# Performance work log

Measured on AMD Instinct MI355X. Metric: run time of the kernel, lower is better.

Reference implementation:

```python
import jax, jax.numpy as jnp
import numpy as np
from jax import lax
jax.config.update("jax_enable_x64", True)

FNV_OFF = np.int64(-3750763034362895579)
FNV_PRIME = np.int64(4294967731)
I64_MAX = np.iinfo(np.int64).max
INF = np.float32(1e38)
CHUNK = 512  # cluster-chunk size for the cdist fallback


def _pack_key(b, c, vx, vy, vz):
    # five-word FNV-1a 64-bit hash with natural int64 wraparound
    h = jnp.full(b.shape, FNV_OFF, dtype=jnp.int64)
    for w in (b, c, vx, vy, vz):
        h = (h ^ w.astype(jnp.int64)) * FNV_PRIME
    return h


def _safe_norm(x):
    s = jnp.sum(x * x, axis=1)
    n = jnp.sqrt(jnp.where(s > 0, s, 1.0))
    return jnp.where(s > 0, n, 0.0)


def setup_inputs() -> dict:
    key = jax.random.key(0)
    k1, k2, k3, k4 = jax.random.split(key, 4)
    N = 65536
    grid = jax.random.randint(k1, (N, 3), 0, 400).astype(jnp.float32)
    batch_id = jnp.sort(jax.random.randint(k2, (N,), 0, 2).astype(jnp.int64))
    label = jax.random.randint(k3, (N,), 0, 8).astype(jnp.int64)
    pred_off = jax.random.normal(k4, (N, 3), dtype=jnp.float32)
    return {"pred_off": pred_off, "grid": grid, "label": label, "batch_id": batch_id,
            "base_grid": 16, "num_cls": 8, "num_batch": 2}


def _forward(pred_off, grid, label, batch_id, base_grid, num_cls, num_batch):
    N = grid.shape[0]
    grid_f = grid.astype(jnp.float32)
    vox = jnp.floor(grid_f / base_grid).astype(jnp.int64)  # [N,3]

    # voxel_grid: bucket by (batch, voxel) -> consecutive cluster ids via unique
    ckey = ((batch_id * 1024 + vox[:, 0]) * 1024 + vox[:, 1]) * 1024 + vox[:, 2]
    _, cluster = jnp.unique(ckey, return_inverse=True, size=N, fill_value=I64_MAX)
    cluster = cluster.reshape(-1)

    # cluster stats (segment scatter-reduce, num_segments = N upper bound)
    cnt = jax.ops.segment_sum(jnp.ones((N,), jnp.float32), cluster, num_segments=N)
    cl_center = jax.ops.segment_sum(grid_f, cluster, num_segments=N) / jnp.maximum(cnt, 1.0)[:, None]
    cl_batch = jax.ops.segment_min(batch_id, cluster, num_segments=N)
    cl_lbl_lo = jax.ops.segment_min(label, cluster, num_segments=N)
    cl_lbl_hi = jax.ops.segment_max(label, cluster, num_segments=N)
    cl_vox = jax.ops.segment_min(vox, cluster, num_segments=N)
    valid_cl = cnt > 0
    pure_cl = (cl_lbl_lo == cl_lbl_hi) & valid_cl
    pure_pt = pure_cl[cluster]

    # hash table of pure clusters, sorted by key (invalid -> sentinel, sorts last)
    pk_all = jnp.where(pure_cl, _pack_key(cl_batch, cl_lbl_lo, cl_vox[:, 0], cl_vox[:, 1], cl_vox[:, 2]), I64_MAX)
    order = jnp.argsort(pk_all)
    pk_sort = pk_all[order]
    pc_sort = cl_center[order]
    ok_sort = pure_cl[order]

    # per (batch,label) global centers
    key_bl = batch_id * num_cls + label
    nbl = num_batch * num_cls
    cnt_bl = jax.ops.segment_sum(jnp.ones((N,), jnp.float32), key_bl, num_segments=nbl)
    global_c = jax.ops.segment_sum(grid_f, key_bl, num_segments=nbl) / jnp.maximum(cnt_bl, 1.0)[:, None]
    step_sign = jnp.sign(global_c[key_bl] - cl_center[cluster]).astype(jnp.int64)  # [N,3]

    # +/-1 and +/-2 voxel hash lookup (steps 1 and K+1=2)
    def probe(step):
        cv = cl_vox[cluster] + step_sign * step
        ck = _pack_key(batch_id, label, cv[:, 0], cv[:, 1], cv[:, 2])
        idx = jnp.searchsorted(pk_sort, ck)
        idxc = jnp.minimum(idx, N - 1)
        hit = (idx < N) & ok_sort[idxc] & (pk_sort[idxc] == ck)
        return hit, pc_sort[idxc]

    hit1, t1 = probe(1)
    hit2, t2 = probe(2)
    hit_pt = hit1 | hit2
    tgt_c = jnp.where(hit1[:, None], t1, jnp.where(hit2[:, None], t2, grid_f))

    # fallback: nearest pure-cluster center with same (batch,label), chunked cdist+argmin
    miss = (~pure_pt) & (~hit_pt)
    code_y = key_bl
    code_x = jnp.where(pure_cl, cl_batch * num_cls + cl_lbl_lo, jnp.int64(-1))
    p2 = jnp.sum(grid_f * grid_f, axis=1)  # [N]

    def body(carry, i):
        best_d, best_c = carry
        c = lax.dynamic_slice_in_dim(cl_center, i * CHUNK, CHUNK)   # [S,3]
        cc = lax.dynamic_slice_in_dim(code_x, i * CHUNK, CHUNK)      # [S]
        d2 = p2[:, None] - 2.0 * (grid_f @ c.T) + jnp.sum(c * c, axis=1)[None, :]  # [N,S]
        d2 = jnp.where(cc[None, :] == code_y[:, None], d2, INF)
        j = jnp.argmin(d2, axis=1)
        dmin = jnp.take_along_axis(d2, j[:, None], axis=1)[:, 0]
        upd = dmin < best_d
        best_d = jnp.where(upd, dmin, best_d)
        best_c = jnp.where(upd[:, None], c[j], best_c)
        return (best_d, best_c), None

    nchunk = N // CHUNK
    (best_d, best_c), _ = lax.scan(body, (jnp.full((N,), INF, jnp.float32), grid_f), jnp.arange(nchunk))
    tgt_c = jnp.where((miss & (best_d < INF))[:, None], best_c, tgt_c)

    # loss: smooth-L1 on offsets below 99th-percentile magnitude + direction cosine loss
    tgt_off = tgt_c - grid_f
    mag = _safe_norm(tgt_off)
    thresh = jnp.quantile(mag, 0.99)
    m1 = mag <= thresh
    d = pred_off - tgt_off
    ad = jnp.abs(d)
    hub = jnp.where(ad < 1.0, 0.5 * d * d, ad - 0.5)
    n1 = jnp.sum(m1).astype(jnp.float32)
    loss_l1 = jnp.where(n1 > 0, jnp.sum(hub * m1[:, None]) / jnp.maximum(n1 * 3.0, 1.0), 0.0)

    md = (mag > 0) & m1
    eps = 1e-4
    pn = _safe_norm(pred_off)
    cos = jnp.sum(pred_off * tgt_off, axis=1) / jnp.maximum(pn * mag, eps)
    nmd = jnp.sum(md).astype(jnp.float32)
    loss_dir = jnp.where(nmd > 0, 1.0 - jnp.sum(cos * md) / jnp.maximum(nmd, 1.0), 0.0)
    return jnp.stack([loss_l1.astype(jnp.float32), loss_dir.astype(jnp.float32)])


def reference(pred_off, grid, label, batch_id, base_grid, num_cls, num_batch):
    return _forward(pred_off, grid, label, batch_id, base_grid, num_cls, num_batch)
```

## Files before the change

### kernel.cpp

```cpp
#include <hip/hip_runtime.h>
#include <climits>

#define VOXD 25
#define SLOT3 (VOXD*VOXD*VOXD)
#define SLOTS (2*SLOT3)
#define NCLS 8
#define NCODE 16
#define NBLK ((SLOTS + 255) / 256)
#define HB 2048
#define FBK 64
#define GSZ 16
#define MPB (256 / GSZ)
#define CSTRIDE SLOT3

struct Scalars {
  double hub;
  double cosSum;
  int n1;
  int nmd;
  int binA, rA, binB, rB;
  float thresh;
  int done;
};

__device__ __forceinline__ int voxslot(int b, int vx, int vy, int vz) {
  return ((b * VOXD + vx) * VOXD + vy) * VOXD + vz;
}

__device__ __forceinline__ int block_scan_i(int v, int* ws, int* total) {
  int lane = threadIdx.x & 63, w = threadIdx.x >> 6;
  int s = v;
  #pragma unroll
  for (int off = 1; off < 64; off <<= 1) {
    int t = __shfl_up(s, off, 64);
    if (lane >= off) s += t;
  }
  if (lane == 63) ws[w] = s;
  __syncthreads();
  if (threadIdx.x < 16) {
    int x = ws[threadIdx.x];
    #pragma unroll
    for (int off = 1; off < 16; off <<= 1) {
      int t = __shfl_up(x, off, 64);
      if (lane >= off) x += t;
    }
    ws[threadIdx.x] = x;
  }
  __syncthreads();
  if (w > 0) s += ws[w - 1];
  *total = ws[15];
  __syncthreads();
  return s;
}

__global__ void k_scatter(const float* __restrict__ grid, const int* __restrict__ label,
                          const int* __restrict__ batch,
                          unsigned long long* vA, unsigned long long* vB, int* lmask,
                          int* blCnt, float* blSum, int n) {
  __shared__ int sCnt[NCODE];
  __shared__ float sSum[3 * NCODE];
  int tid = threadIdx.x;
  if (tid < NCODE) sCnt[tid] = 0;
  if (tid < 3 * NCODE) sSum[tid] = 0.f;
  __syncthreads();
  int i = blockIdx.x * blockDim.x + tid;
  if (i < n) {
    float gx = grid[3*i], gy = grid[3*i+1], gz = grid[3*i+2];
    int ix = (int)gx, iy = (int)gy, iz = (int)gz;
    int vx = (int)floorf(gx * (1.0f/16.0f));
    int vy = (int)floorf(gy * (1.0f/16.0f));
    int vz = (int)floorf(gz * (1.0f/16.0f));
    int b = batch[i], l = label[i];
    int s = voxslot(b, vx, vy, vz);
    atomicAdd(&vA[s], ((unsigned long long)(unsigned)ix << 32) | (unsigned)iy);
    atomicAdd(&vB[s], ((unsigned long long)(unsigned)iz << 24) | 1ULL);
    atomicOr(&lmask[s], 1 << l);
    int bl = b * NCLS + l;
    atomicAdd(&sCnt[bl], 1);
    atomicAdd(&sSum[3*bl], gx); atomicAdd(&sSum[3*bl+1], gy); atomicAdd(&sSum[3*bl+2], gz);
  }
  __syncthreads();
  if (tid < NCODE && sCnt[tid] != 0) atomicAdd(&blCnt[tid], sCnt[tid]);
  if (tid < 3 * NCODE && sSum[tid] != 0.f) atomicAdd(&blSum[tid], sSum[tid]);
}

__global__ void k_prep(const unsigned long long* vA, const unsigned long long* vB,
                       const int* lmask, float4* ctr, float4* pC, int* pSlot,
                       int* codeCnt) {
  __shared__ int lc[NCODE];
  __shared__ int lb[NCODE];
  int tid = threadIdx.x;
  if (tid < NCODE) lc[tid] = 0;
  __syncthreads();
  int s = blockIdx.x * 256 + tid;
  int code = -1, lpos = 0;
  float4 v = make_float4(0.f, 0.f, 0.f, __int_as_float(-2));
  if (s < SLOTS) {
    unsigned long long bq = vB[s];
    unsigned c = (unsigned)(bq & 0xFFFFFFULL);
    if (c > 0) {
      unsigned long long aq = vA[s];
      float fc = (float)c;
      float cx = __fdiv_rn((float)(unsigned)(aq >> 32), fc);
      float cy = __fdiv_rn((float)(unsigned)(aq & 0xFFFFFFFFULL), fc);
      float cz = __fdiv_rn((float)(unsigned)(bq >> 24), fc);
      int m = lmask[s];
      bool pure = (m & (m - 1)) == 0;
      int lbl = __ffs(m) - 1;
      v = make_float4(cx, cy, cz, __int_as_float(pure ? lbl : -1));
      if (pure) {
        code = (s / SLOT3) * NCLS + lbl;
        lpos = atomicAdd(&lc[code], 1);
      }
    }
    ctr[s] = v;
  }
  __syncthreads();
  if (tid < NCODE) lb[tid] = (lc[tid] > 0) ? atomicAdd(&codeCnt[tid], lc[tid]) : 0;
  __syncthreads();
  if (code >= 0) {
    int pos = code * CSTRIDE + lb[code] + lpos;
    float c2 = __fadd_rn(__fadd_rn(__fmul_rn(v.x,v.x), __fmul_rn(v.y,v.y)),
                         __fmul_rn(v.z,v.z));
    pC[pos] = make_float4(v.x, v.y, v.z, c2);
    pSlot[pos] = s;
  }
}

__global__ void k_targets(const float* __restrict__ grid, const int* __restrict__ label,
                          const int* __restrict__ batch,
                          const float4* __restrict__ ctr,
                          const int* __restrict__ blCnt, const float* __restrict__ blSum,
                          float* tgt, float* mag, int* ghist,
                          int* missPart, int* missCnt, int mstride, int n) {
  __shared__ int wCnt[4][NCODE];
  __shared__ int gBase[NCODE];
  __shared__ int h[HB];
  int tid = threadIdx.x, lane = tid & 63, w = tid >> 6;
  for (int t = tid; t < HB; t += 256) h[t] = 0;
  __syncthreads();
  int i = blockIdx.x * blockDim.x + tid;
  bool active = (i < n);
  bool miss = false;
  int mcode = -1;

  if (active) {
    float gx = grid[3*i], gy = grid[3*i+1], gz = grid[3*i+2];
    int vx = (int)floorf(gx * (1.0f/16.0f));
    int vy = (int)floorf(gy * (1.0f/16.0f));
    int vz = (int)floorf(gz * (1.0f/16.0f));
    int b = batch[i], l = label[i];
    int s = voxslot(b, vx, vy, vz);

    float4 own = ctr[s];
    bool purept = (__float_as_int(own.w) >= 0);

    int bl = b * NCLS + l;
    float fbc = (float)max(blCnt[bl], 1);
    float gcx = __fdiv_rn(blSum[3*bl],   fbc);
    float gcy = __fdiv_rn(blSum[3*bl+1], fbc);
    float gcz = __fdiv_rn(blSum[3*bl+2], fbc);

    float dx = __fsub_rn(gcx, own.x);
    float dy = __fsub_rn(gcy, own.y);
    float dz = __fsub_rn(gcz, own.z);
    int sgx = (dx > 0.f) ? 1 : ((dx < 0.f) ? -1 : 0);
    int sgy = (dy > 0.f) ? 1 : ((dy < 0.f) ? -1 : 0);
    int sgz = (dz > 0.f) ? 1 : ((dz < 0.f) ? -1 : 0);

    int ax1 = vx + sgx,     ay1 = vy + sgy,     az1 = vz + sgz;
    int ax2 = vx + 2 * sgx, ay2 = vy + 2 * sgy, az2 = vz + 2 * sgz;
    bool v1 = (unsigned)ax1 < (unsigned)VOXD && (unsigned)ay1 < (unsigned)VOXD &&
              (unsigned)az1 < (unsigned)VOXD;
    bool v2 = (unsigned)ax2 < (unsigned)VOXD && (unsigned)ay2 < (unsigned)VOXD &&
              (unsigned)az2 < (unsigned)VOXD;

    float4 q1 = make_float4(0.f, 0.f, 0.f, __int_as_float(-3));
    float4 q2 = q1;
    if (v1) q1 = ctr[voxslot(b, ax1, ay1, az1)];
    if (v2) q2 = ctr[voxslot(b, ax2, ay2, az2)];

    bool hit1 = v1 && (__float_as_int(q1.w) == l);
    bool hit2 = v2 && (__float_as_int(q2.w) == l);
    bool hit = hit1 || hit2;

    float tx = hit1 ? q1.x : (hit2 ? q2.x : gx);
    float ty = hit1 ? q1.y : (hit2 ? q2.y : gy);
    float tz = hit1 ? q1.z : (hit2 ? q2.z : gz);

    tgt[3*i] = tx; tgt[3*i+1] = ty; tgt[3*i+2] = tz;
    miss = (!purept && !hit);
    if (miss) {
      mcode = bl;
    } else {
      float tox = __fsub_rn(tx, gx), toy = __fsub_rn(ty, gy), toz = __fsub_rn(tz, gz);
      float ssq = __fadd_rn(__fadd_rn(__fmul_rn(tox,tox), __fmul_rn(toy,toy)),
                            __fmul_rn(toz,toz));
      float m = (ssq > 0.f) ? sqrtf(ssq) : 0.f;
      mag[i] = m;
      atomicAdd(&h[__float_as_uint(m) >> 21], 1);
    }
  }
  int myrank = 0;
  #pragma unroll
  for (int c = 0; c < NCODE; ++c) {
    unsigned long long mb = __ballot(mcode == c);
    if (lane == 0) wCnt[w][c] = __popcll(mb);
    if (mcode == c) myrank = __popcll(mb & ((1ULL << lane) - 1ULL));
  }
  __syncthreads();
  if (tid < NCODE) {
    int tot = wCnt[0][tid] + wCnt[1][tid] + wCnt[2][tid] + wCnt[3][tid];
    gBase[tid] = (tot > 0) ? atomicAdd(&missCnt[tid], tot) : 0;
  }
  __syncthreads();
  if (miss) {
    int base = gBase[mcode];
    for (int q = 0; q < 4; ++q) if (q < w) base += wCnt[q][mcode];
    missPart[mcode * mstride + base + myrank] = i;
  }
  for (int t = tid; t < HB; t += 256) {
    int c = h[t];
    if (c != 0) atomicAdd(&ghist[t], c);
  }
}

__global__ void __launch_bounds__(256) k_fallback(
    const float* __restrict__ grid,
    const float4* __restrict__ pC, const int* __restrict__ pSlot,
    const float4* __restrict__ ctr,
    const int* __restrict__ codeCnt,
    const int* __restrict__ missPart, const int* __restrict__ missCnt,
    float* tgt, float* mag, int* ghist, int mstride) {
  __shared__ float4 tile[1024];
  __shared__ int stile[1024];
  __shared__ int h[HB];
  int c = blockIdx.x / FBK;
  int y = blockIdx.x % FBK;
  int mc = missCnt[c];
  if (y * MPB >= mc) return;
  int cc = codeCnt[c];
  int j0 = c * CSTRIDE;
  const int* mlist = missPart + c * mstride;
  int g = threadIdx.x >> 4;
  int q = threadIdx.x & (GSZ - 1);
  for (int t = threadIdx.x; t < HB; t += 256) h[t] = 0;

  for (int base = y * MPB; base < mc; base += FBK * MPB) {
    int t = base + g;
    bool valid = (t < mc);
    int idx = 0;
    float gx = 0.f, gy = 0.f, gz = 0.f, p2 = 0.f;
    if (valid) {
      idx = mlist[t];
      gx = grid[3*idx]; gy = grid[3*idx+1]; gz = grid[3*idx+2];
      p2 = __fadd_rn(__fadd_rn(__fmul_rn(gx,gx), __fmul_rn(gy,gy)), __fmul_rn(gz,gz));
    }
    unsigned long long key = 0xFFFFFFFFFFFFFFFFULL;
    for (int tb = 0; tb < cc; tb += 1024) {
      int m = min(1024, cc - tb);
      __syncthreads();
      for (int j = threadIdx.x; j < m; j += 256) {
        tile[j] = pC[j0 + tb + j];
        stile[j] = pSlot[j0 + tb + j];
      }
      __syncthreads();
      if (valid) {
        #pragma unroll 4
        for (int j = q; j < m; j += GSZ) {
          float4 cl = tile[j];
          float dot = __fadd_rn(__fadd_rn(__fmul_rn(gx,cl.x), __fmul_rn(gy,cl.y)),
                                __fmul_rn(gz,cl.z));
          float d2 = __fadd_rn(__fsub_rn(p2, __fmul_rn(2.0f, dot)), cl.w);
          unsigned fb = __float_as_uint(d2);
          fb = (fb >> 31) ? ~fb : (fb | 0x80000000u);
          unsigned long long k2 = ((unsigned long long)fb << 32) | (unsigned)stile[j];
          if (k2 < key) key = k2;
        }
      }
    }
    #pragma unroll
    for (int off = 1; off < GSZ; off <<= 1) {
      unsigned long long o = __shfl_xor(key, off, 64);
      if (o < key) key = o;
    }
    if (valid && q == 0) {
      float m = 0.f;
      if (cc > 0) {
        int slot = (int)(unsigned)(key & 0xFFFFFFFFULL);
        float4 cl = ctr[slot];
        tgt[3*idx] = cl.x; tgt[3*idx+1] = cl.y; tgt[3*idx+2] = cl.z;
        float tox = __fsub_rn(cl.x, gx), toy = __fsub_rn(cl.y, gy), toz = __fsub_rn(cl.z, gz);
        float ssq = __fadd_rn(__fadd_rn(__fmul_rn(tox,tox), __fmul_rn(toy,toy)),
                              __fmul_rn(toz,toz));
        m = (ssq > 0.f) ? sqrtf(ssq) : 0.f;
      }
      mag[idx] = m;
      atomicAdd(&h[__float_as_uint(m) >> 21], 1);
    }
    __syncthreads();
  }
  for (int t = threadIdx.x; t < HB; t += 256) {
    int cv = h[t];
    if (cv != 0) atomicAdd(&ghist[t], cv);
  }
}

__global__ void k_gather(const float* __restrict__ mag, const int* __restrict__ ghist,
                         Scalars* sc, unsigned* bufA, unsigned* bufB, int* cntAB,
                         int n, int r0, int r1) {
  __shared__ int ws[4];
  __shared__ int sBinA, sRA, sBinB, sRB;
  int tid = threadIdx.x, lane = tid & 63, w = tid >> 6;
  int base8 = tid * 8;
  int cbin[8];
  int s = 0;
  #pragma unroll
  for (int k = 0; k < 8; ++k) { cbin[k] = ghist[base8 + k]; s += cbin[k]; }
  int incl = s;
  #pragma unroll
  for (int off = 1; off < 64; off <<= 1) {
    int t = __shfl_up(incl, off, 64);
    if (lane >= off) incl += t;
  }
  if (lane == 63) ws[w] = incl;
  __syncthreads();
  int wofs = 0;
  #pragma unroll
  for (int qq = 0; qq < 4; ++qq) if (qq < w) wofs += ws[qq];
  int lo = wofs + incl - s;
  if (r0 >= lo && r0 < lo + s) {
    int acc = lo;
    #pragma unroll
    for (int k = 0; k < 8; ++k) {
      if (r0 < acc + cbin[k]) { sBinA = base8 + k; sRA = r0 - acc; break; }
      acc += cbin[k];
    }
  }
  if (r1 >= lo && r1 < lo + s) {
    int acc = lo;
    #pragma unroll
    for (int k = 0; k < 8; ++k) {
      if (r1 < acc + cbin[k]) { sBinB = base8 + k; sRB = r1 - acc; break; }
      acc += cbin[k];
    }
  }
  __syncthreads();
  if (blockIdx.x == 0 && tid == 0) {
    sc->binA = sBinA; sc->rA = sRA; sc->binB = sBinB; sc->rB = sRB;
  }
  int binA = sBinA, binB = sBinB;

  int i = blockIdx.x * blockDim.x + tid;
  unsigned bits = 0;
  bool inA = false, inB = false;
  if (i < n) {
    bits = __float_as_uint(mag[i]);
    unsigned cb = bits >> 21;
    inA = (cb == (unsigned)binA);
    inB = (cb == (unsigned)binB);
  }
  {
    unsigned long long mb = __ballot(inA);
    int mc = __popcll(mb);
    int bs = 0;
    if (lane == 0 && mc > 0) bs = atomicAdd(&cntAB[0], mc);
    bs = __shfl(bs, 0, 64);
    if (inA) bufA[bs + __popcll(mb & ((1ULL << lane) - 1ULL))] = bits;
  }
  {
    unsigned long long mb = __ballot(inB);
    int mc = __popcll(mb);
    int bs = 0;
    if (lane == 0 && mc > 0) bs = atomicAdd(&cntAB[1], mc);
    bs = __shfl(bs, 0, 64);
    if (inB) bufB[bs + __popcll(mb & ((1ULL << lane) - 1ULL))] = bits;
  }
}

__device__ unsigned select_in_bin(const unsigned* __restrict__ buf, int cnt,
                                  int coarse, int rank, int* h, int* ws) {
  __shared__ int sSub, sSubR, sLow;
  for (int t = threadIdx.x; t < HB; t += 1024) h[t] = 0;
  __syncthreads();
  for (int t = threadIdx.x; t < cnt; t += 1024)
    atomicAdd(&h[(buf[t] >> 10) & 0x7FF], 1);
  __syncthreads();
  int t = threadIdx.x;
  int s0 = h[2*t], s1 = h[2*t+1];
  int tot;
  int incl = block_scan_i(s0 + s1, ws, &tot);
  int b1 = incl - s1, b0 = b1 - s0;
  if (rank >= b0 && rank < b0 + s0) { sSub = 2*t;   sSubR = rank - b0; }
  if (rank >= b1 && rank < b1 + s1) { sSub = 2*t+1; sSubR = rank - b1; }
  __syncthreads();
  int subv = sSub, subr = sSubR;
  h[t] = 0;
  __syncthreads();
  for (int q = threadIdx.x; q < cnt; q += 1024) {
    unsigned v = buf[q];
    if ((int)((v >> 10) & 0x7FF) == subv) atomicAdd(&h[v & 0x3FF], 1);
  }
  __syncthreads();
  int c = h[t];
  int tot2;
  int incl2 = block_scan_i(c, ws, &tot2);
  int lb = incl2 - c;
  if (subr >= lb && subr < lb + c) sLow = t;
  __syncthreads();
  return ((unsigned)coarse << 21) | ((unsigned)subv << 10) | (unsigned)sLow;
}

__global__ void __launch_bounds__(1024) k_sel(const unsigned* __restrict__ bufA,
                                              const unsigned* __restrict__ bufB,
                                              const int* __restrict__ cntAB,
                                              Scalars* sc, double tfrac) {
  __shared__ int h[HB];
  __shared__ int ws[16];
  unsigned va = select_in_bin(bufA, cntAB[0], sc->binA, sc->rA, h, ws);
  __syncthreads();
  unsigned vb = select_in_bin(bufB, cntAB[1], sc->binB, sc->rB, h, ws);
  if (threadIdx.x == 0) {
    double a = (double)__uint_as_float(va);
    double b = (double)__uint_as_float(vb);
    double th = (tfrac >= 0.5) ? (b - (b - a) * (1.0 - tfrac)) : (a + (b - a) * tfrac);
    sc->thresh = (float)th;
  }
}

__global__ void k_loss(const float* __restrict__ pred, const float* __restrict__ grid,
                       const float* __restrict__ tgt, const float* __restrict__ mag,
                       Scalars* sc, float* out, int n) {
  __shared__ double shH[256];
  __shared__ double shC[256];
  __shared__ int shN[256];
  __shared__ int shM[256];
  int tid = threadIdx.x;
  int i = blockIdx.x * blockDim.x + tid;
  double hub = 0.0, cs = 0.0;
  int c1 = 0, cmd = 0;
  if (i < n) {
    float th = sc->thresh;
    float m = mag[i];
    if (m <= th) {
      c1 = 1;
      float tox = __fsub_rn(tgt[3*i],   grid[3*i]);
      float toy = __fsub_rn(tgt[3*i+1], grid[3*i+1]);
      float toz = __fsub_rn(tgt[3*i+2], grid[3*i+2]);
      float px = pred[3*i], py = pred[3*i+1], pz = pred[3*i+2];
      float d0 = __fsub_rn(px, tox), d1 = __fsub_rn(py, toy), d2 = __fsub_rn(pz, toz);
      float a0 = fabsf(d0), a1 = fabsf(d1), a2 = fabsf(d2);
      float h0 = (a0 < 1.f) ? __fmul_rn(__fmul_rn(0.5f, d0), d0) : __fsub_rn(a0, 0.5f);
      float h1 = (a1 < 1.f) ? __fmul_rn(__fmul_rn(0.5f, d1), d1) : __fsub_rn(a1, 0.5f);
      float h2 = (a2 < 1.f) ? __fmul_rn(__fmul_rn(0.5f, d2), d2) : __fsub_rn(a2, 0.5f);
      hub = (double)h0 + (double)h1 + (double)h2;
      if (m > 0.f) {
        cmd = 1;
        float ps = __fadd_rn(__fadd_rn(__fmul_rn(px,px), __fmul_rn(py,py)), __fmul_rn(pz,pz));
        float pn = (ps > 0.f) ? sqrtf(ps) : 0.f;
        float dotp = __fadd_rn(__fadd_rn(__fmul_rn(px,tox), __fmul_rn(py,toy)),
                               __fmul_rn(pz,toz));
        float den = fmaxf(__fmul_rn(pn, m), 1e-4f);
        cs = (double)__fdiv_rn(dotp, den);
      }
    }
  }
  shH[tid] = hub; shC[tid] = cs; shN[tid] = c1; shM[tid] = cmd;
  __syncthreads();
  for (int off = 128; off > 0; off >>= 1) {
    if (tid < off) {
      shH[tid] += shH[tid+off];
      shC[tid] += shC[tid+off];
      shN[tid] += shN[tid+off];
      shM[tid] += shM[tid+off];
    }
    __syncthreads();
  }
  if (tid == 0) {
    atomicAdd(&sc->hub, shH[0]);
    atomicAdd(&sc->cosSum, shC[0]);
    atomicAdd(&sc->n1, shN[0]);
    atomicAdd(&sc->nmd, shM[0]);
    __threadfence();
    int d = atomicAdd(&sc->done, 1);
    if (d == (int)gridDim.x - 1) {
      __threadfence();
      double th_hub = atomicAdd(&sc->hub, 0.0);
      double th_cos = atomicAdd(&sc->cosSum, 0.0);
      int n1 = atomicAdd(&sc->n1, 0);
      int nmd = atomicAdd(&sc->nmd, 0);
      double l1 = (n1 > 0) ? th_hub / fmax((double)n1 * 3.0, 1.0) : 0.0;
      double ld = (nmd > 0) ? (1.0 - th_cos / fmax((double)nmd, 1.0)) : 0.0;
      out[0] = (float)l1;
      out[1] = (float)ld;
    }
  }
}

extern "C" void kernel_launch(void* const* d_in, const int* in_sizes, int n_in,
                              void* d_out, int out_size, void* d_ws, size_t ws_size,
                              hipStream_t stream) {
  const float* pred  = (const float*)d_in[0];
  const float* grid  = (const float*)d_in[1];
  const int*   label = (const int*)d_in[2];
  const int*   batch = (const int*)d_in[3];
  int n = in_sizes[2];
  int mstride = n / 4;

  char* p = (char*)d_ws;
  auto take = [&](size_t bytes) -> char* {
    char* r = p;
    p += (bytes + 255) & ~(size_t)255;
    return r;
  };
  char* zbase = p;
  unsigned long long* vA = (unsigned long long*)take((size_t)SLOTS*8);
  unsigned long long* vB = (unsigned long long*)take((size_t)SLOTS*8);
  int*    lmask    = (int*)   take((size_t)SLOTS*4);
  int*    codeCnt  = (int*)   take(NCODE*4);
  int*    missCnt  = (int*)   take(NCODE*4);
  int*    blCnt    = (int*)   take(16*4);
  float*  blSum    = (float*) take(48*4);
  int*    cntAB    = (int*)   take(2*4);
  int*    ghist    = (int*)   take((size_t)HB*4);
  Scalars* sc      = (Scalars*)take(sizeof(Scalars));
  size_t zbytes = (size_t)(p - zbase);
  float4* ctr      = (float4*)take((size_t)SLOTS*16);
  float4* pC       = (float4*)take((size_t)NCODE*CSTRIDE*16);
  int*    pSlot    = (int*)   take((size_t)NCODE*CSTRIDE*4);
  unsigned* bufA   = (unsigned*)take((size_t)n*4);
  unsigned* bufB   = (unsigned*)take((size_t)n*4);
  float*  tgt      = (float*) take((size_t)n*3*4);
  float*  mag      = (float*) take((size_t)n*4);
  int*    missPart = (int*)   take((size_t)NCODE*mstride*4);

  int nb = (n + 255) / 256;

  double vi = 0.99 * (double)(n - 1);
  int r0 = (int)vi;
  int r1 = r0 + 1; if (r1 > n - 1) r1 = n - 1;
  double tfrac = vi - (double)r0;

  hipMemsetAsync(zbase, 0, zbytes, stream);
  k_scatter<<<nb, 256, 0, stream>>>(grid, label, batch, vA, vB, lmask,
                                    blCnt, blSum, n);
  k_prep<<<NBLK, 256, 0, stream>>>(vA, vB, lmask, ctr, pC, pSlot, codeCnt);
  k_targets<<<nb, 256, 0, stream>>>(grid, label, batch, ctr, blCnt, blSum,
                                    tgt, mag, ghist, missPart, missCnt, mstride, n);
  k_fallback<<<NCODE * FBK, 256, 0, stream>>>(grid, pC, pSlot, ctr, codeCnt,
                                              missPart, missCnt, tgt, mag, ghist,
                                              mstride);
  k_gather<<<nb, 256, 0, stream>>>(mag, ghist, sc, bufA, bufB, cntAB, n, r0, r1);
  k_sel<<<1, 1024, 0, stream>>>(bufA, bufB, cntAB, sc, tfrac);
  k_loss<<<nb, 256, 0, stream>>>(pred, grid, tgt, mag, sc, (float*)d_out, n);
}
```

Before: 163.7 us.

## Fuse fallback search into targets kernel and redundantly compute quantile select per block

Merges the miss-list building and the nearest-cluster fallback into the targets kernel, so each block handles its own misses from shared memory instead of going through a global miss partition and a separate launch. It also folds the histogram gather, the single-block radix select and the loss into one kernel, where every block rescans the whole mag array to rebuild the sub-bin histograms. This cuts the launch count from seven to four and drops the global scratch buffers. In exchange, each of the 256 loss blocks reads all N magnitudes twice, and blocks with misses may load cluster tiles repeatedly with uneven load.

```diff
diff --git a/kernel.cpp b/kernel.cpp
--- a/kernel.cpp
+++ b/kernel.cpp
@@ -8,9 +8,7 @@
 #define NCODE 16
 #define NBLK ((SLOTS + 255) / 256)
 #define HB 2048
-#define FBK 64
 #define GSZ 16
-#define MPB (256 / GSZ)
 #define CSTRIDE SLOT3
 
 struct Scalars {
@@ -18,7 +16,6 @@
   double cosSum;
   int n1;
   int nmd;
-  int binA, rA, binB, rB;
   float thresh;
   int done;
 };
@@ -27,7 +24,7 @@
   return ((b * VOXD + vx) * VOXD + vy) * VOXD + vz;
 }
 
-__device__ __forceinline__ int block_scan_i(int v, int* ws, int* total) {
+__device__ __forceinline__ int block_scan256(int v, int* ws) {
   int lane = threadIdx.x & 63, w = threadIdx.x >> 6;
   int s = v;
   #pragma unroll
@@ -37,20 +34,11 @@
   }
   if (lane == 63) ws[w] = s;
   __syncthreads();
-  if (threadIdx.x < 16) {
-    int x = ws[threadIdx.x];
-    #pragma unroll
-    for (int off = 1; off < 16; off <<= 1) {
-      int t = __shfl_up(x, off, 64);
-      if (lane >= off) x += t;
-    }
-    ws[threadIdx.x] = x;
-  }
-  __syncthreads();
-  if (w > 0) s += ws[w - 1];
-  *total = ws[15];
-  __syncthreads();
-  return s;
+  int add = 0;
+  #pragma unroll
+  for (int q = 0; q < 4; ++q) if (q < w) add += ws[q];
+  __syncthreads();
+  return s + add;
 }
 
 __global__ void k_scatter(const float* __restrict__ grid, const int* __restrict__ label,
@@ -127,25 +115,35 @@
   }
 }
 
-__global__ void k_targets(const float* __restrict__ grid, const int* __restrict__ label,
-                          const int* __restrict__ batch,
-                          const float4* __restrict__ ctr,
-                          const int* __restrict__ blCnt, const float* __restrict__ blSum,
-                          float* tgt, float* mag, int* ghist,
-                          int* missPart, int* missCnt, int mstride, int n) {
-  __shared__ int wCnt[4][NCODE];
-  __shared__ int gBase[NCODE];
+__global__ void __launch_bounds__(256) k_targets_fb(
+    const float* __restrict__ grid, const int* __restrict__ label,
+    const int* __restrict__ batch,
+    const float4* __restrict__ ctr,
+    const int* __restrict__ blCnt, const float* __restrict__ blSum,
+    const float4* __restrict__ pC, const int* __restrict__ pSlot,
+    const int* __restrict__ codeCnt,
+    float* tgt, float* mag, int* ghist, int n) {
   __shared__ int h[HB];
-  int tid = threadIdx.x, lane = tid & 63, w = tid >> 6;
+  __shared__ float4 mpt[256];
+  __shared__ int midx[256];
+  __shared__ unsigned long long bestk[256];
+  __shared__ int cnt16[NCODE];
+  __shared__ int mofs[NCODE];
+  __shared__ float4 tile[1024];
+  __shared__ int stile[1024];
+
+  int tid = threadIdx.x;
   for (int t = tid; t < HB; t += 256) h[t] = 0;
-  __syncthreads();
+  if (tid < NCODE) cnt16[tid] = 0;
+  __syncthreads();
+
   int i = blockIdx.x * blockDim.x + tid;
-  bool active = (i < n);
   bool miss = false;
   int mcode = -1;
-
-  if (active) {
-    float gx = grid[3*i], gy = grid[3*i+1], gz = grid[3*i+2];
+  float gx = 0.f, gy = 0.f, gz = 0.f;
+
+  if (i < n) {
+    gx = grid[3*i]; gy = grid[3*i+1]; gz = grid[3*i+2];
     int vx = (int)floorf(gx * (1.0f/16.0f));
     int vy = (int)floorf(gy * (1.0f/16.0f));
     int vz = (int)floorf(gz * (1.0f/16.0f));
@@ -201,139 +199,119 @@
       atomicAdd(&h[__float_as_uint(m) >> 21], 1);
     }
   }
-  int myrank = 0;
-  #pragma unroll
+
+  int lpos = -1;
+  if (miss) lpos = atomicAdd(&cnt16[mcode], 1);
+  __syncthreads();
+  if (tid == 0) {
+    int acc = 0;
+    #pragma unroll
+    for (int c = 0; c < NCODE; ++c) { mofs[c] = acc; acc += cnt16[c]; }
+  }
+  __syncthreads();
+  if (miss) {
+    int pos = mofs[mcode] + lpos;
+    midx[pos] = i;
+    float p2 = __fadd_rn(__fadd_rn(__fmul_rn(gx,gx), __fmul_rn(gy,gy)),
+                         __fmul_rn(gz,gz));
+    mpt[pos] = make_float4(gx, gy, gz, p2);
+  }
+  __syncthreads();
+
+  int g = tid >> 4;
+  int q = tid & (GSZ - 1);
   for (int c = 0; c < NCODE; ++c) {
-    unsigned long long mb = __ballot(mcode == c);
-    if (lane == 0) wCnt[w][c] = __popcll(mb);
-    if (mcode == c) myrank = __popcll(mb & ((1ULL << lane) - 1ULL));
-  }
-  __syncthreads();
-  if (tid < NCODE) {
-    int tot = wCnt[0][tid] + wCnt[1][tid] + wCnt[2][tid] + wCnt[3][tid];
-    gBase[tid] = (tot > 0) ? atomicAdd(&missCnt[tid], tot) : 0;
-  }
-  __syncthreads();
-  if (miss) {
-    int base = gBase[mcode];
-    for (int q = 0; q < 4; ++q) if (q < w) base += wCnt[q][mcode];
-    missPart[mcode * mstride + base + myrank] = i;
-  }
-  for (int t = tid; t < HB; t += 256) {
-    int c = h[t];
-    if (c != 0) atomicAdd(&ghist[t], c);
-  }
-}
-
-__global__ void __launch_bounds__(256) k_fallback(
-    const float* __restrict__ grid,
-    const float4* __restrict__ pC, const int* __restrict__ pSlot,
-    const float4* __restrict__ ctr,
-    const int* __restrict__ codeCnt,
-    const int* __restrict__ missPart, const int* __restrict__ missCnt,
-    float* tgt, float* mag, int* ghist, int mstride) {
-  __shared__ float4 tile[1024];
-  __shared__ int stile[1024];
-  __shared__ int h[HB];
-  int c = blockIdx.x / FBK;
-  int y = blockIdx.x % FBK;
-  int mc = missCnt[c];
-  if (y * MPB >= mc) return;
-  int cc = codeCnt[c];
-  int j0 = c * CSTRIDE;
-  const int* mlist = missPart + c * mstride;
-  int g = threadIdx.x >> 4;
-  int q = threadIdx.x & (GSZ - 1);
-  for (int t = threadIdx.x; t < HB; t += 256) h[t] = 0;
-
-  for (int base = y * MPB; base < mc; base += FBK * MPB) {
-    int t = base + g;
-    bool valid = (t < mc);
-    int idx = 0;
-    float gx = 0.f, gy = 0.f, gz = 0.f, p2 = 0.f;
-    if (valid) {
-      idx = mlist[t];
-      gx = grid[3*idx]; gy = grid[3*idx+1]; gz = grid[3*idx+2];
-      p2 = __fadd_rn(__fadd_rn(__fmul_rn(gx,gx), __fmul_rn(gy,gy)), __fmul_rn(gz,gz));
-    }
-    unsigned long long key = 0xFFFFFFFFFFFFFFFFULL;
+    int mc = cnt16[c];
+    if (mc == 0) continue;
+    int cc = codeCnt[c];
+    int j0 = c * CSTRIDE;
+    int off = mofs[c];
+    for (int t = tid; t < mc; t += 256) bestk[off + t] = 0xFFFFFFFFFFFFFFFFULL;
+    __syncthreads();
     for (int tb = 0; tb < cc; tb += 1024) {
       int m = min(1024, cc - tb);
-      __syncthreads();
-      for (int j = threadIdx.x; j < m; j += 256) {
+      for (int j = tid; j < m; j += 256) {
         tile[j] = pC[j0 + tb + j];
         stile[j] = pSlot[j0 + tb + j];
       }
       __syncthreads();
-      if (valid) {
+      for (int t = g; t < mc; t += GSZ) {
+        float4 pp = mpt[off + t];
+        unsigned long long key = 0xFFFFFFFFFFFFFFFFULL;
         #pragma unroll 4
         for (int j = q; j < m; j += GSZ) {
           float4 cl = tile[j];
-          float dot = __fadd_rn(__fadd_rn(__fmul_rn(gx,cl.x), __fmul_rn(gy,cl.y)),
-                                __fmul_rn(gz,cl.z));
-          float d2 = __fadd_rn(__fsub_rn(p2, __fmul_rn(2.0f, dot)), cl.w);
+          float dot = __fadd_rn(__fadd_rn(__fmul_rn(pp.x,cl.x), __fmul_rn(pp.y,cl.y)),
+                                __fmul_rn(pp.z,cl.z));
+          float d2 = __fadd_rn(__fsub_rn(pp.w, __fmul_rn(2.0f, dot)), cl.w);
           unsigned fb = __float_as_uint(d2);
           fb = (fb >> 31) ? ~fb : (fb | 0x80000000u);
           unsigned long long k2 = ((unsigned long long)fb << 32) | (unsigned)stile[j];
           if (k2 < key) key = k2;
         }
+        #pragma unroll
+        for (int o = 1; o < GSZ; o <<= 1) {
+          unsigned long long ok = __shfl_xor(key, o, 64);
+          if (ok < key) key = ok;
+        }
+        if (q == 0 && key < bestk[off + t]) bestk[off + t] = key;
       }
-    }
-    #pragma unroll
-    for (int off = 1; off < GSZ; off <<= 1) {
-      unsigned long long o = __shfl_xor(key, off, 64);
-      if (o < key) key = o;
-    }
-    if (valid && q == 0) {
-      float m = 0.f;
+      __syncthreads();
+    }
+    for (int t = tid; t < mc; t += 256) {
+      unsigned long long key = bestk[off + t];
+      int idx = midx[off + t];
+      float4 pp = mpt[off + t];
+      float mv = 0.f;
       if (cc > 0) {
         int slot = (int)(unsigned)(key & 0xFFFFFFFFULL);
         float4 cl = ctr[slot];
         tgt[3*idx] = cl.x; tgt[3*idx+1] = cl.y; tgt[3*idx+2] = cl.z;
-        float tox = __fsub_rn(cl.x, gx), toy = __fsub_rn(cl.y, gy), toz = __fsub_rn(cl.z, gz);
+        float tox = __fsub_rn(cl.x, pp.x), toy = __fsub_rn(cl.y, pp.y),
+              toz = __fsub_rn(cl.z, pp.z);
         float ssq = __fadd_rn(__fadd_rn(__fmul_rn(tox,tox), __fmul_rn(toy,toy)),
                               __fmul_rn(toz,toz));
-        m = (ssq > 0.f) ? sqrtf(ssq) : 0.f;
+        mv = (ssq > 0.f) ? sqrtf(ssq) : 0.f;
       }
-      mag[idx] = m;
-      atomicAdd(&h[__float_as_uint(m) >> 21], 1);
+      mag[idx] = mv;
+      atomicAdd(&h[__float_as_uint(mv) >> 21], 1);
     }
     __syncthreads();
   }
-  for (int t = threadIdx.x; t < HB; t += 256) {
+
+  for (int t = tid; t < HB; t += 256) {
     int cv = h[t];
     if (cv != 0) atomicAdd(&ghist[t], cv);
   }
 }
 
-__global__ void k_gather(const float* __restrict__ mag, const int* __restrict__ ghist,
-                         Scalars* sc, unsigned* bufA, unsigned* bufB, int* cntAB,
-                         int n, int r0, int r1) {
+__global__ void __launch_bounds__(256) k_loss_sel(
+    const float* __restrict__ pred, const float* __restrict__ grid,
+    const float* __restrict__ tgt, const float* __restrict__ mag,
+    const int* __restrict__ ghist, Scalars* sc, float* out,
+    int n, int r0, int r1, double tfrac) {
+  __shared__ int histA[HB];
+  __shared__ int histB[HB];
   __shared__ int ws[4];
-  __shared__ int sBinA, sRA, sBinB, sRB;
-  int tid = threadIdx.x, lane = tid & 63, w = tid >> 6;
+  __shared__ int s_misc[8];
+  __shared__ double shH[256];
+  __shared__ double shC[256];
+  __shared__ int shN[256];
+  __shared__ int shM[256];
+  int tid = threadIdx.x;
+
   int base8 = tid * 8;
   int cbin[8];
   int s = 0;
   #pragma unroll
   for (int k = 0; k < 8; ++k) { cbin[k] = ghist[base8 + k]; s += cbin[k]; }
-  int incl = s;
-  #pragma unroll
-  for (int off = 1; off < 64; off <<= 1) {
-    int t = __shfl_up(incl, off, 64);
-    if (lane >= off) incl += t;
-  }
-  if (lane == 63) ws[w] = incl;
-  __syncthreads();
-  int wofs = 0;
-  #pragma unroll
-  for (int qq = 0; qq < 4; ++qq) if (qq < w) wofs += ws[qq];
-  int lo = wofs + incl - s;
+  int incl = block_scan256(s, ws);
+  int lo = incl - s;
   if (r0 >= lo && r0 < lo + s) {
     int acc = lo;
     #pragma unroll
     for (int k = 0; k < 8; ++k) {
-      if (r0 < acc + cbin[k]) { sBinA = base8 + k; sRA = r0 - acc; break; }
+      if (r0 < acc + cbin[k]) { s_misc[0] = base8 + k; s_misc[1] = r0 - acc; break; }
       acc += cbin[k];
     }
   }
@@ -341,106 +319,129 @@
     int acc = lo;
     #pragma unroll
     for (int k = 0; k < 8; ++k) {
-      if (r1 < acc + cbin[k]) { sBinB = base8 + k; sRB = r1 - acc; break; }
+      if (r1 < acc + cbin[k]) { s_misc[2] = base8 + k; s_misc[3] = r1 - acc; break; }
       acc += cbin[k];
     }
   }
   __syncthreads();
-  if (blockIdx.x == 0 && tid == 0) {
-    sc->binA = sBinA; sc->rA = sRA; sc->binB = sBinB; sc->rB = sRB;
-  }
-  int binA = sBinA, binB = sBinB;
-
-  int i = blockIdx.x * blockDim.x + tid;
-  unsigned bits = 0;
-  bool inA = false, inB = false;
-  if (i < n) {
-    bits = __float_as_uint(mag[i]);
-    unsigned cb = bits >> 21;
-    inA = (cb == (unsigned)binA);
-    inB = (cb == (unsigned)binB);
-  }
+  int binA = s_misc[0], rA = s_misc[1], binB = s_misc[2], rB = s_misc[3];
+
+  for (int t = tid; t < HB; t += 256) { histA[t] = 0; histB[t] = 0; }
+  __syncthreads();
   {
-    unsigned long long mb = __ballot(inA);
-    int mc = __popcll(mb);
-    int bs = 0;
-    if (lane == 0 && mc > 0) bs = atomicAdd(&cntAB[0], mc);
-    bs = __shfl(bs, 0, 64);
-    if (inA) bufA[bs + __popcll(mb & ((1ULL << lane) - 1ULL))] = bits;
-  }
+    const uint4* m4 = (const uint4*)mag;
+    int nv = n >> 2;
+    for (int v = tid; v < nv; v += 256) {
+      uint4 u = m4[v];
+      unsigned b0 = u.x, b1 = u.y, b2 = u.z, b3 = u.w;
+      if ((b0 >> 21) == (unsigned)binA) atomicAdd(&histA[(b0 >> 10) & 0x7FF], 1);
+      if ((b0 >> 21) == (unsigned)binB) atomicAdd(&histB[(b0 >> 10) & 0x7FF], 1);
+      if ((b1 >> 21) == (unsigned)binA) atomicAdd(&histA[(b1 >> 10) & 0x7FF], 1);
+      if ((b1 >> 21) == (unsigned)binB) atomicAdd(&histB[(b1 >> 10) & 0x7FF], 1);
+      if ((b2 >> 21) == (unsigned)binA) atomicAdd(&histA[(b2 >> 10) & 0x7FF], 1);
+      if ((b2 >> 21) == (unsigned)binB) atomicAdd(&histB[(b2 >> 10) & 0x7FF], 1);
+      if ((b3 >> 21) == (unsigned)binA) atomicAdd(&histA[(b3 >> 10) & 0x7FF], 1);
+      if ((b3 >> 21) == (unsigned)binB) atomicAdd(&histB[(b3 >> 10) & 0x7FF], 1);
+    }
+    for (int t = (nv << 2) + tid; t < n; t += 256) {
+      unsigned b0 = __float_as_uint(mag[t]);
+      if ((b0 >> 21) == (unsigned)binA) atomicAdd(&histA[(b0 >> 10) & 0x7FF], 1);
+      if ((b0 >> 21) == (unsigned)binB) atomicAdd(&histB[(b0 >> 10) & 0x7FF], 1);
+    }
+  }
+  __syncthreads();
+
   {
-    unsigned long long mb = __ballot(inB);
-    int mc = __popcll(mb);
-    int bs = 0;
-    if (lane == 0 && mc > 0) bs = atomicAdd(&cntAB[1], mc);
-    bs = __shfl(bs, 0, 64);
-    if (inB) bufB[bs + __popcll(mb & ((1ULL << lane) - 1ULL))] = bits;
-  }
-}
-
-__device__ unsigned select_in_bin(const unsigned* __restrict__ buf, int cnt,
-                                  int coarse, int rank, int* h, int* ws) {
-  __shared__ int sSub, sSubR, sLow;
-  for (int t = threadIdx.x; t < HB; t += 1024) h[t] = 0;
-  __syncthreads();
-  for (int t = threadIdx.x; t < cnt; t += 1024)
-    atomicAdd(&h[(buf[t] >> 10) & 0x7FF], 1);
-  __syncthreads();
-  int t = threadIdx.x;
-  int s0 = h[2*t], s1 = h[2*t+1];
-  int tot;
-  int incl = block_scan_i(s0 + s1, ws, &tot);
-  int b1 = incl - s1, b0 = b1 - s0;
-  if (rank >= b0 && rank < b0 + s0) { sSub = 2*t;   sSubR = rank - b0; }
-  if (rank >= b1 && rank < b1 + s1) { sSub = 2*t+1; sSubR = rank - b1; }
-  __syncthreads();
-  int subv = sSub, subr = sSubR;
-  h[t] = 0;
-  __syncthreads();
-  for (int q = threadIdx.x; q < cnt; q += 1024) {
-    unsigned v = buf[q];
-    if ((int)((v >> 10) & 0x7FF) == subv) atomicAdd(&h[v & 0x3FF], 1);
-  }
-  __syncthreads();
-  int c = h[t];
-  int tot2;
-  int incl2 = block_scan_i(c, ws, &tot2);
-  int lb = incl2 - c;
-  if (subr >= lb && subr < lb + c) sLow = t;
-  __syncthreads();
-  return ((unsigned)coarse << 21) | ((unsigned)subv << 10) | (unsigned)sLow;
-}
-
-__global__ void __launch_bounds__(1024) k_sel(const unsigned* __restrict__ bufA,
-                                              const unsigned* __restrict__ bufB,
-                                              const int* __restrict__ cntAB,
-                                              Scalars* sc, double tfrac) {
-  __shared__ int h[HB];
-  __shared__ int ws[16];
-  unsigned va = select_in_bin(bufA, cntAB[0], sc->binA, sc->rA, h, ws);
-  __syncthreads();
-  unsigned vb = select_in_bin(bufB, cntAB[1], sc->binB, sc->rB, h, ws);
-  if (threadIdx.x == 0) {
+    int a8[8], sA = 0;
+    #pragma unroll
+    for (int k = 0; k < 8; ++k) { a8[k] = histA[base8 + k]; sA += a8[k]; }
+    int inclA = block_scan256(sA, ws);
+    int accA = inclA - sA;
+    #pragma unroll
+    for (int k = 0; k < 8; ++k) {
+      if (rA >= accA && rA < accA + a8[k]) { s_misc[4] = base8 + k; s_misc[5] = rA - accA; }
+      accA += a8[k];
+    }
+    int b8[8], sB = 0;
+    #pragma unroll
+    for (int k = 0; k < 8; ++k) { b8[k] = histB[base8 + k]; sB += b8[k]; }
+    int inclB = block_scan256(sB, ws);
+    int accB = inclB - sB;
+    #pragma unroll
+    for (int k = 0; k < 8; ++k) {
+      if (rB >= accB && rB < accB + b8[k]) { s_misc[6] = base8 + k; s_misc[7] = rB - accB; }
+      accB += b8[k];
+    }
+  }
+  __syncthreads();
+  int subA = s_misc[4], subRA = s_misc[5], subB = s_misc[6], subRB = s_misc[7];
+
+  for (int t = tid; t < 1024; t += 256) { histA[t] = 0; histB[t] = 0; }
+  __syncthreads();
+  {
+    const uint4* m4 = (const uint4*)mag;
+    int nv = n >> 2;
+    for (int v = tid; v < nv; v += 256) {
+      uint4 u = m4[v];
+      unsigned bb[4] = { u.x, u.y, u.z, u.w };
+      #pragma unroll
+      for (int k = 0; k < 4; ++k) {
+        unsigned b0 = bb[k];
+        if ((b0 >> 21) == (unsigned)binA && (int)((b0 >> 10) & 0x7FF) == subA)
+          atomicAdd(&histA[b0 & 0x3FF], 1);
+        if ((b0 >> 21) == (unsigned)binB && (int)((b0 >> 10) & 0x7FF) == subB)
+          atomicAdd(&histB[b0 & 0x3FF], 1);
+      }
+    }
+    for (int t = (nv << 2) + tid; t < n; t += 256) {
+      unsigned b0 = __float_as_uint(mag[t]);
+      if ((b0 >> 21) == (unsigned)binA && (int)((b0 >> 10) & 0x7FF) == subA)
+        atomicAdd(&histA[b0 & 0x3FF], 1);
+      if ((b0 >> 21) == (unsigned)binB && (int)((b0 >> 10) & 0x7FF) == subB)
+        atomicAdd(&histB[b0 & 0x3FF], 1);
+    }
+  }
+  __syncthreads();
+
+  {
+    int base4 = tid * 4;
+    int la[4], sA = 0;
+    #pragma unroll
+    for (int k = 0; k < 4; ++k) { la[k] = histA[base4 + k]; sA += la[k]; }
+    int inclA = block_scan256(sA, ws);
+    int accA = inclA - sA;
+    #pragma unroll
+    for (int k = 0; k < 4; ++k) {
+      if (subRA >= accA && subRA < accA + la[k]) s_misc[0] = base4 + k;
+      accA += la[k];
+    }
+    int lb4[4], sB = 0;
+    #pragma unroll
+    for (int k = 0; k < 4; ++k) { lb4[k] = histB[base4 + k]; sB += lb4[k]; }
+    int inclB = block_scan256(sB, ws);
+    int accB = inclB - sB;
+    #pragma unroll
+    for (int k = 0; k < 4; ++k) {
+      if (subRB >= accB && subRB < accB + lb4[k]) s_misc[1] = base4 + k;
+      accB += lb4[k];
+    }
+  }
+  __syncthreads();
+  unsigned va = ((unsigned)binA << 21) | ((unsigned)subA << 10) | (unsigned)s_misc[0];
+  unsigned vb = ((unsigned)binB << 21) | ((unsigned)subB << 10) | (unsigned)s_misc[1];
+  float th;
+  {
     double a = (double)__uint_as_float(va);
     double b = (double)__uint_as_float(vb);
-    double th = (tfrac >= 0.5) ? (b - (b - a) * (1.0 - tfrac)) : (a + (b - a) * tfrac);
-    sc->thresh = (float)th;
-  }
-}
-
-__global__ void k_loss(const float* __restrict__ pred, const float* __restrict__ grid,
-                       const float* __restrict__ tgt, const float* __restrict__ mag,
-                       Scalars* sc, float* out, int n) {
-  __shared__ double shH[256];
-  __shared__ double shC[256];
-  __shared__ int shN[256];
-  __shared__ int shM[256];
-  int tid = threadIdx.x;
+    double thd = (tfrac >= 0.5) ? (b - (b - a) * (1.0 - tfrac)) : (a + (b - a) * tfrac);
+    th = (float)thd;
+  }
+  __syncthreads();
+
   int i = blockIdx.x * blockDim.x + tid;
   double hub = 0.0, cs = 0.0;
   int c1 = 0, cmd = 0;
   if (i < n) {
-    float th = sc->thresh;
     float m = mag[i];
     if (m <= th) {
       c1 = 1;
@@ -505,7 +506,6 @@
   const int*   label = (const int*)d_in[2];
   const int*   batch = (const int*)d_in[3];
   int n = in_sizes[2];
-  int mstride = n / 4;
 
   char* p = (char*)d_ws;
   auto take = [&](size_t bytes) -> char* {
@@ -518,21 +518,16 @@
   unsigned long long* vB = (unsigned long long*)take((size_t)SLOTS*8);
   int*    lmask    = (int*)   take((size_t)SLOTS*4);
   int*    codeCnt  = (int*)   take(NCODE*4);
-  int*    missCnt  = (int*)   take(NCODE*4);
   int*    blCnt    = (int*)   take(16*4);
   float*  blSum    = (float*) take(48*4);
-  int*    cntAB    = (int*)   take(2*4);
   int*    ghist    = (int*)   take((size_t)HB*4);
   Scalars* sc      = (Scalars*)take(sizeof(Scalars));
   size_t zbytes = (size_t)(p - zbase);
   float4* ctr      = (float4*)take((size_t)SLOTS*16);
   float4* pC       = (float4*)take((size_t)NCODE*CSTRIDE*16);
   int*    pSlot    = (int*)   take((size_t)NCODE*CSTRIDE*4);
-  unsigned* bufA   = (unsigned*)take((size_t)n*4);
-  unsigned* bufB   = (unsigned*)take((size_t)n*4);
   float*  tgt      = (float*) take((size_t)n*3*4);
   float*  mag      = (float*) take((size_t)n*4);
-  int*    missPart = (int*)   take((size_t)NCODE*mstride*4);
 
   int nb = (n + 255) / 256;
 
@@ -545,12 +540,8 @@
   k_scatter<<<nb, 256, 0, stream>>>(grid, label, batch, vA, vB, lmask,
                                     blCnt, blSum, n);
   k_prep<<<NBLK, 256, 0, stream>>>(vA, vB, lmask, ctr, pC, pSlot, codeCnt);
-  k_targets<<<nb, 256, 0, stream>>>(grid, label, batch, ctr, blCnt, blSum,
-                                    tgt, mag, ghist, missPart, missCnt, mstride, n);
-  k_fallback<<<NCODE * FBK, 256, 0, stream>>>(grid, pC, pSlot, ctr, codeCnt,
-                                              missPart, missCnt, tgt, mag, ghist,
-                                              mstride);
-  k_gather<<<nb, 256, 0, stream>>>(mag, ghist, sc, bufA, bufB, cntAB, n, r0, r1);
-  k_sel<<<1, 1024, 0, stream>>>(bufA, bufB, cntAB, sc, tfrac);
-  k_loss<<<nb, 256, 0, stream>>>(pred, grid, tgt, mag, sc, (float*)d_out, n);
-}
+  k_targets_fb<<<nb, 256, 0, stream>>>(grid, label, batch, ctr, blCnt, blSum,
+                                       pC, pSlot, codeCnt, tgt, mag, ghist, n);
+  k_loss_sel<<<nb, 256, 0, stream>>>(pred, grid, tgt, mag, ghist, sc,
+                                     (float*)d_out, n, r0, r1, tfrac);
+}
```

Measured after the change: 221.3 us. +35.2%, slower.
